# Kernel tuning notes

Hardware: AMD Instinct MI355X
Metric: run time of the kernel (lower is better)

The kernel has to match this reference:

```python
import jax, jax.numpy as jnp
import numpy as np

D_MODEL = 2048
N_HEADS = 16
QK_HEAD_DIM = D_MODEL // N_HEADS  # 128
V_HEAD_DIM = 128
KV_LORA_RANK = 512
EPS = 1e-6
B, S = 2, 2048
ROPE_THETA = 10000.0


def setup_inputs() -> dict:
    key = jax.random.key(0)
    ks = jax.random.split(key, 7)
    x = jax.random.normal(ks[0], (B, S, D_MODEL), dtype=jnp.float32)
    # RoPE frequencies: freqs_cis[s, i] = exp(1j * s * theta^(-2i/d)) -> cos/sin
    inv_freq = 1.0 / (ROPE_THETA ** (np.arange(0, QK_HEAD_DIM, 2, dtype=np.float32) / QK_HEAD_DIM))
    ang = np.arange(S, dtype=np.float32)[:, None] * inv_freq[None, :]  # [S, 64]
    freqs_cos = jnp.asarray(np.cos(ang), dtype=jnp.float32)
    freqs_sin = jnp.asarray(np.sin(ang), dtype=jnp.float32)
    # Parameters stored as [in, out] so that y = x @ W
    def lin(k, fan_in, fan_out):
        return jax.random.normal(k, (fan_in, fan_out), dtype=jnp.float32) / np.sqrt(fan_in)
    w_kv_compress = lin(ks[1], D_MODEL, KV_LORA_RANK)
    kv_norm_w = jnp.ones((KV_LORA_RANK,), dtype=jnp.float32)
    w_k_up = lin(ks[2], KV_LORA_RANK, N_HEADS * QK_HEAD_DIM)
    w_v_up = lin(ks[3], KV_LORA_RANK, N_HEADS * V_HEAD_DIM)
    w_q = lin(ks[4], D_MODEL, N_HEADS * QK_HEAD_DIM)
    w_out = lin(ks[5], N_HEADS * V_HEAD_DIM, D_MODEL)
    return {"x": x, "freqs_cos": freqs_cos, "freqs_sin": freqs_sin,
            "w_kv_compress": w_kv_compress, "kv_norm_w": kv_norm_w,
            "w_k_up": w_k_up, "w_v_up": w_v_up, "w_q": w_q, "w_out": w_out}


def _rms_norm(x, w, eps=EPS):
    var = jnp.mean(jnp.square(x), axis=-1, keepdims=True)
    return x * jax.lax.rsqrt(var + eps) * w


def _apply_rope(t, cos, sin):
    # t: [B, S, H, D]; cos/sin: [S, D//2]; pairs are adjacent elements (complex view)
    b, s, h, d = t.shape
    tr = t.reshape(b, s, h, d // 2, 2)
    x1, x2 = tr[..., 0], tr[..., 1]
    c = cos[None, :, None, :]
    sn = sin[None, :, None, :]
    o1 = x1 * c - x2 * sn
    o2 = x1 * sn + x2 * c
    return jnp.stack([o1, o2], axis=-1).reshape(b, s, h, d)


def reference(x, freqs_cos, freqs_sin, w_kv_compress, kv_norm_w, w_k_up, w_v_up, w_q, w_out):
    b, s, _ = x.shape
    kv_latent = _rms_norm(x @ w_kv_compress, kv_norm_w)      # [B,S,R]
    k = (kv_latent @ w_k_up).reshape(b, s, N_HEADS, QK_HEAD_DIM)
    v = (kv_latent @ w_v_up).reshape(b, s, N_HEADS, V_HEAD_DIM)
    q = (x @ w_q).reshape(b, s, N_HEADS, QK_HEAD_DIM)
    q = _apply_rope(q, freqs_cos, freqs_sin)
    k = _apply_rope(k, freqs_cos, freqs_sin)
    scale = 1.0 / np.sqrt(QK_HEAD_DIM)
    scores = jnp.einsum('bqhd,bkhd->bhqk', q, k) * scale     # [B,H,S,S]
    causal = jnp.tril(jnp.ones((s, s), dtype=bool))
    scores = jnp.where(causal[None, None], scores, jnp.finfo(scores.dtype).min)
    probs = jax.nn.softmax(scores, axis=-1)
    attn = jnp.einsum('bhqk,bkhd->bqhd', probs, v)           # [B,S,H,Dv]
    out = attn.reshape(b, s, N_HEADS * V_HEAD_DIM) @ w_out   # [B,S,d_model]
    return out
```

## Files before the change

### kernel.cpp

```cpp
#include <hip/hip_runtime.h>

typedef unsigned short u16;
typedef __attribute__((ext_vector_type(8))) short bf16x8;
typedef __attribute__((ext_vector_type(4))) float floatx4;

__device__ __forceinline__ float bf2f(u16 h) {
  return __uint_as_float(((unsigned int)h) << 16);
}
__device__ __forceinline__ u16 f2bf(float f) {
  unsigned int u = __float_as_uint(f);
  u += 0x7fffu + ((u >> 16) & 1u);
  return (u16)(u >> 16);
}
__device__ __forceinline__ u16 f2bf_hu(float f) {
  return (u16)((__float_as_uint(f) + 0x8000u) >> 16);
}
__device__ __forceinline__ float exp2fast(float x) {
  float r;
  asm("v_exp_f32 %0, %1" : "=v"(r) : "v"(x));
  return r;
}
__device__ __forceinline__ bool is_f32(const u16* probe) { return probe[0] == 0; }

#define GLOAD_LDS16(gsrc, ldst)                                                        \
  __builtin_amdgcn_global_load_lds(                                                    \
      (const __attribute__((address_space(1))) unsigned int*)(gsrc),                   \
      (__attribute__((address_space(3))) unsigned int*)(ldst), 16, 0, 0)

__global__ __launch_bounds__(256) void cvt_to_bf16(const void* __restrict__ in,
                                                   u16* __restrict__ out, int n,
                                                   const u16* __restrict__ probe) {
  int i = (blockIdx.x * 256 + threadIdx.x) * 8;
  if (i >= n) return;
  if (is_f32(probe)) {
    const float* f = (const float*)in;
    uint4 o;
    o.x = (unsigned)f2bf(f[i + 0]) | ((unsigned)f2bf(f[i + 1]) << 16);
    o.y = (unsigned)f2bf(f[i + 2]) | ((unsigned)f2bf(f[i + 3]) << 16);
    o.z = (unsigned)f2bf(f[i + 4]) | ((unsigned)f2bf(f[i + 5]) << 16);
    o.w = (unsigned)f2bf(f[i + 6]) | ((unsigned)f2bf(f[i + 7]) << 16);
    *(uint4*)(out + i) = o;
  } else {
    *(uint4*)(out + i) = *(const uint4*)((const u16*)in + i);
  }
}

__global__ __launch_bounds__(256) void transpose_cvt(const void* __restrict__ in,
                                                     u16* __restrict__ out,
                                                     int R, int C,
                                                     const u16* __restrict__ probe) {
  __shared__ u16 tile[32][33];
  int bx = blockIdx.x * 32;
  int by = blockIdx.y * 32;
  int tx = threadIdx.x & 31, ty = threadIdx.x >> 5;
  if (is_f32(probe)) {
    const float* f = (const float*)in;
    for (int i = 0; i < 32; i += 8)
      tile[ty + i][tx] = f2bf(f[(size_t)(by + ty + i) * C + (bx + tx)]);
  } else {
    const u16* u = (const u16*)in;
    for (int i = 0; i < 32; i += 8)
      tile[ty + i][tx] = u[(size_t)(by + ty + i) * C + (bx + tx)];
  }
  __syncthreads();
  for (int i = 0; i < 32; i += 8)
    out[(size_t)(bx + ty + i) * R + (by + tx)] = tile[tx][ty + i];
}

__global__ __launch_bounds__(512, 2) void gemm8(const u16* __restrict__ A,
                                                const u16* __restrict__ BT,
                                                void* __restrict__ Ca, int sa,
                                                u16* __restrict__ Cb, int sb,
                                                int N, int K, int nsplit, int mode,
                                                const u16* __restrict__ fc,
                                                const u16* __restrict__ fs,
                                                float oscale,
                                                const u16* __restrict__ probe) {
  extern __shared__ __align__(16) u16 ldsbuf[];
  u16* const AsB = ldsbuf;
  u16* const BsB = ldsbuf + 32768;
#define ASLOT(b, k) (AsB + ((((b) << 1) | (k)) << 13))
#define BSLOT(b, k) (BsB + ((((b) << 1) | (k)) << 13))

  const int t = threadIdx.x;
  const int lane = t & 63, wid = t >> 6;
  const int quad = lane >> 4, l16 = lane & 15;
  const int wr = wid >> 2, wc = wid & 3;
  const int m0 = blockIdx.y * 256, n0 = blockIdx.x * 256;
  const int NT = K >> 6;

  const u16* const Abase = A + (size_t)m0 * K;
  const u16* const Bbase = BT + (size_t)n0 * K;

  const int e0 = t, e1 = 512 + t;
  const int r0 = e0 >> 2, r1 = e1 >> 2;
  const int sg0 = (e0 & 3) ^ ((r0 & 3) ^ ((r0 >> 2) & 3));
  const int sg1 = (e1 & 3) ^ ((r1 & 3) ^ ((r1 >> 2) & 3));
  const u16* const sa0 = Abase + (size_t)r0 * K + sg0 * 8;
  const u16* const sa1 = Abase + (size_t)r1 * K + sg1 * 8;
  const u16* const sb0 = Bbase + (size_t)r0 * K + sg0 * 8;
  const u16* const sb1 = Bbase + (size_t)r1 * K + sg1 * 8;
#define STAGE_A(slot, kb)                      \
  do {                                         \
    GLOAD_LDS16(sa0 + (kb), (slot) + e0 * 8);  \
    GLOAD_LDS16(sa1 + (kb), (slot) + e1 * 8);  \
  } while (0)
#define STAGE_B(slot, kb)                      \
  do {                                         \
    GLOAD_LDS16(sb0 + (kb), (slot) + e0 * 8);  \
    GLOAD_LDS16(sb1 + (kb), (slot) + e1 * 8);  \
  } while (0)

  const int gofs = (quad ^ ((l16 & 3) ^ ((l16 >> 2) & 3))) * 8;
#define FRAG(slot, row) (*(const bf16x8*)((slot) + (row) * 32 + gofs))

#define SYNC_MID()                                          \
  __builtin_amdgcn_s_barrier();                             \
  asm volatile("s_waitcnt lgkmcnt(0)" ::: "memory");        \
  __builtin_amdgcn_sched_barrier(0)

  floatx4 acc[8][4];
#pragma unroll
  for (int i = 0; i < 8; ++i)
#pragma unroll
    for (int j = 0; j < 4; ++j) acc[i][j] = (floatx4){0.f, 0.f, 0.f, 0.f};

  STAGE_A(ASLOT(0, 0), 0);
  STAGE_B(BSLOT(0, 0), 0);
  STAGE_A(ASLOT(0, 1), 32);
  STAGE_B(BSLOT(0, 1), 32);
  STAGE_A(ASLOT(1, 0), 64);
  STAGE_B(BSLOT(1, 0), 64);
  asm volatile("s_waitcnt vmcnt(4)" ::: "memory");
  __builtin_amdgcn_s_barrier();

  bf16x8 af[4], bfr[4];
  const int arow = wr * 128 + l16;
  const int brow = wc * 64 + l16;

#pragma unroll 1
  for (int u = 0; u < NT; ++u) {
    const int cur = u & 1, oth = cur ^ 1;
    u16* const A0 = ASLOT(cur, 0);
    u16* const A1 = ASLOT(cur, 1);
    u16* const B0 = BSLOT(cur, 0);
    u16* const B1 = BSLOT(cur, 1);
    const bool s1 = (u + 1 < NT), s2 = (u + 2 < NT);
    const int kb1 = (u + 1) << 6, kb2 = (u + 2) << 6;

#pragma unroll
    for (int mi = 0; mi < 4; ++mi) af[mi] = FRAG(A0, arow + mi * 16);
#pragma unroll
    for (int nj = 0; nj < 4; ++nj) bfr[nj] = FRAG(B0, brow + nj * 16);
    if (s1) STAGE_A(ASLOT(oth, 1), kb1 + 32);
    SYNC_MID();
    __builtin_amdgcn_s_setprio(1);
#pragma unroll
    for (int mi = 0; mi < 4; ++mi)
#pragma unroll
      for (int nj = 0; nj < 4; ++nj)
        acc[mi][nj] = __builtin_amdgcn_mfma_f32_16x16x32_bf16(af[mi], bfr[nj], acc[mi][nj], 0, 0, 0);
    __builtin_amdgcn_s_setprio(0);
    __builtin_amdgcn_sched_barrier(0);
    __builtin_amdgcn_s_barrier();

#pragma unroll
    for (int mi = 0; mi < 4; ++mi) af[mi] = FRAG(A0, arow + 64 + mi * 16);
    if (s1) STAGE_B(BSLOT(oth, 1), kb1 + 32);
    SYNC_MID();
    __builtin_amdgcn_s_setprio(1);
#pragma unroll
    for (int mi = 0; mi < 4; ++mi)
#pragma unroll
      for (int nj = 0; nj < 4; ++nj)
        acc[mi + 4][nj] = __builtin_amdgcn_mfma_f32_16x16x32_bf16(af[mi], bfr[nj], acc[mi + 4][nj], 0, 0, 0);
    __builtin_amdgcn_s_setprio(0);
    __builtin_amdgcn_sched_barrier(0);
    if (u == NT - 1) asm volatile("s_waitcnt vmcnt(0)" ::: "memory");
    __builtin_amdgcn_s_barrier();

#pragma unroll
    for (int mi = 0; mi < 4; ++mi) af[mi] = FRAG(A1, arow + mi * 16);
#pragma unroll
    for (int nj = 0; nj < 4; ++nj) bfr[nj] = FRAG(B1, brow + nj * 16);
    if (s2) STAGE_A(A0, kb2);
    SYNC_MID();
    __builtin_amdgcn_s_setprio(1);
#pragma unroll
    for (int mi = 0; mi < 4; ++mi)
#pragma unroll
      for (int nj = 0; nj < 4; ++nj)
        acc[mi][nj] = __builtin_amdgcn_mfma_f32_16x16x32_bf16(af[mi], bfr[nj], acc[mi][nj], 0, 0, 0);
    __builtin_amdgcn_s_setprio(0);
    __builtin_amdgcn_sched_barrier(0);
    __builtin_amdgcn_s_barrier();

#pragma unroll
    for (int mi = 0; mi < 4; ++mi) af[mi] = FRAG(A1, arow + 64 + mi * 16);
    if (s2) STAGE_B(B0, kb2);
    SYNC_MID();
    __builtin_amdgcn_s_setprio(1);
#pragma unroll
    for (int mi = 0; mi < 4; ++mi)
#pragma unroll
      for (int nj = 0; nj < 4; ++nj)
        acc[mi + 4][nj] = __builtin_amdgcn_mfma_f32_16x16x32_bf16(af[mi], bfr[nj], acc[mi + 4][nj], 0, 0, 0);
    __builtin_amdgcn_s_setprio(0);
    __builtin_amdgcn_sched_barrier(0);
    asm volatile("s_waitcnt vmcnt(4)" ::: "memory");
    __builtin_amdgcn_s_barrier();
  }

  if (mode == 0) {
    const bool f32o = is_f32(probe);
#pragma unroll
    for (int mi = 0; mi < 8; ++mi) {
      int rbase = m0 + wr * 128 + mi * 16 + quad * 4;
#pragma unroll
      for (int nj = 0; nj < 4; ++nj) {
        int col = n0 + wc * 64 + nj * 16 + l16;
        if (f32o) {
          float* Cf = (float*)Ca;
          for (int r = 0; r < 4; ++r) Cf[(size_t)(rbase + r) * sa + col] = acc[mi][nj][r];
        } else {
          u16* Ch = (u16*)Ca;
          for (int r = 0; r < 4; ++r) Ch[(size_t)(rbase + r) * sa + col] = f2bf(acc[mi][nj][r]);
        }
      }
    }
  } else if (n0 < nsplit) {
    const bool odd = (l16 & 1);
    u16* Ch = (u16*)Ca;
#pragma unroll
    for (int mi = 0; mi < 8; ++mi) {
      int rbase = m0 + wr * 128 + mi * 16 + quad * 4;
#pragma unroll
      for (int nj = 0; nj < 4; ++nj) {
        int col = n0 + wc * 64 + nj * 16 + l16;
        int p = (col & 127) >> 1;
        for (int r = 0; r < 4; ++r) {
          int srow = (rbase + r) & 2047;
          float c = bf2f(fc[srow * 64 + p]);
          float sn = bf2f(fs[srow * 64 + p]);
          float v = acc[mi][nj][r];
          float pv = __shfl_xor(v, 1);
          float o = fmaf(v, c, odd ? pv * sn : -pv * sn);
          Ch[(size_t)(rbase + r) * sa + col] = f2bf(o * oscale);
        }
      }
    }
  } else if (mode == 1) {
#pragma unroll
    for (int mi = 0; mi < 8; ++mi) {
      int rbase = m0 + wr * 128 + mi * 16 + quad * 4;
#pragma unroll
      for (int nj = 0; nj < 4; ++nj) {
        int col = n0 - nsplit + wc * 64 + nj * 16 + l16;
        for (int r = 0; r < 4; ++r)
          Cb[(size_t)(rbase + r) * sb + col] = f2bf(acc[mi][nj][r]);
      }
    }
  } else {
#pragma unroll
    for (int mi = 0; mi < 8; ++mi) {
      int token0 = m0 + wr * 128 + mi * 16 + quad * 4;
#pragma unroll
      for (int nj = 0; nj < 4; ++nj) {
        int ch = n0 - nsplit + wc * 64 + nj * 16 + l16;
        size_t base = (((size_t)((token0 >> 11) * 16 + (ch >> 7)) * 128 + (ch & 127)) << 11) +
                      (token0 & 2047);
        ushort4 pk;
        pk.x = f2bf(acc[mi][nj][0]);
        pk.y = f2bf(acc[mi][nj][1]);
        pk.z = f2bf(acc[mi][nj][2]);
        pk.w = f2bf(acc[mi][nj][3]);
        *(ushort4*)(Cb + base) = pk;
      }
    }
  }
#undef ASLOT
#undef BSLOT
#undef STAGE_A
#undef STAGE_B
#undef FRAG
#undef SYNC_MID
}

__global__ __launch_bounds__(256) void rmsnorm_kernel(u16* __restrict__ t,
                                                      const u16* __restrict__ w) {
  int row = blockIdx.x * 4 + (threadIdx.x >> 6);
  int lane = threadIdx.x & 63;
  u16* xr = t + (size_t)row * 512;
  float v[8];
  float ss = 0.f;
  for (int i = 0; i < 8; ++i) {
    v[i] = bf2f(xr[lane + i * 64]);
    ss += v[i] * v[i];
  }
  for (int d = 32; d > 0; d >>= 1) ss += __shfl_xor(ss, d);
  float r = rsqrtf(ss * (1.f / 512.f) + 1e-6f);
  for (int i = 0; i < 8; ++i) xr[lane + i * 64] = f2bf(v[i] * r * bf2f(w[lane + i * 64]));
}

__global__ __launch_bounds__(256) void attn_kernel(const u16* __restrict__ q,
                                                   const u16* __restrict__ k,
                                                   const u16* __restrict__ vt,
                                                   u16* __restrict__ o) {
  const int S = 2048;
  __shared__ __align__(16) u16 Kt[64 * 128];
  __shared__ __align__(16) u16 Vt[128 * 64];
  __shared__ __align__(16) u16 P[4][16][64];
  const int t = threadIdx.x;
  const int w = t >> 6, lane = t & 63;
  const int quad = lane >> 4, l16 = lane & 15;
  const int bh = blockIdx.x;
  const int b = bh >> 4, h = bh & 15;
  const int qb = (int)gridDim.y - 1 - (int)blockIdx.y;
  const int q0 = qb * 64 + w * 16;

  const u16* qbase = q + ((size_t)(b * S + q0 + l16)) * 2048 + h * 128;
  bf16x8 qf[4];
  for (int c = 0; c < 4; ++c) qf[c] = *(const bf16x8*)(qbase + c * 32 + quad * 8);

  const u16* kbase = k + (size_t)b * S * 2048 + h * 128;
  const u16* vtb = vt + (size_t)bh * 128 * S;

  const int ksrow = t >> 4, ksc = t & 15;
  const int vsrow = t >> 3, vsc = t & 7;

  bf16x8 onesf;
#pragma unroll
  for (int i = 0; i < 8; ++i) onesf[i] = (short)0x3F80;

  float m_i[4], l_i[4];
  floatx4 acc[8];
  for (int r = 0; r < 4; ++r) { m_i[r] = -1e30f; l_i[r] = 0.f; }
  for (int nd = 0; nd < 8; ++nd) acc[nd] = (floatx4){0.f, 0.f, 0.f, 0.f};

  const int kmax = q0 + 15;
  const int qbase64 = qb * 64;
  for (int kb = 0; kb <= qbase64; kb += 64) {
    const bool diag = (kb == qbase64);
    __syncthreads();
    for (int j = 0; j < 4; ++j) {
      int row = j * 16 + ksrow;
      GLOAD_LDS16(kbase + (size_t)(kb + row) * 2048 + (ksc ^ (row & 15)) * 8,
                  Kt + (size_t)(row * 16 + ksc) * 8);
    }
    for (int j = 0; j < 4; ++j) {
      int row = j * 32 + vsrow;
      GLOAD_LDS16(vtb + (size_t)row * S + kb + ((vsc ^ (row & 7)) * 8),
                  Vt + (size_t)(row * 8 + vsc) * 8);
    }
    __syncthreads();

    floatx4 s[4];
    if (!diag) {
      for (int ns = 0; ns < 4; ++ns) {
        s[ns] = (floatx4){0.f, 0.f, 0.f, 0.f};
        for (int c = 0; c < 4; ++c) {
          bf16x8 kf = *(const bf16x8*)&Kt[(ns * 16 + l16) * 128 + ((c * 4 + quad) ^ l16) * 8];
          s[ns] = __builtin_amdgcn_mfma_f32_16x16x32_bf16(qf[c], kf, s[ns], 0, 0, 0);
        }
      }
    } else {
      for (int ns = 0; ns < 4; ++ns) {
        if (kb + ns * 16 <= kmax) {
          s[ns] = (floatx4){0.f, 0.f, 0.f, 0.f};
          for (int c = 0; c < 4; ++c) {
            bf16x8 kf = *(const bf16x8*)&Kt[(ns * 16 + l16) * 128 + ((c * 4 + quad) ^ l16) * 8];
            s[ns] = __builtin_amdgcn_mfma_f32_16x16x32_bf16(qf[c], kf, s[ns], 0, 0, 0);
          }
          int key = kb + ns * 16 + l16;
          for (int r = 0; r < 4; ++r)
            s[ns][r] = (key > q0 + quad * 4 + r) ? -1e30f : s[ns][r];
        } else {
          s[ns] = (floatx4){-1e30f, -1e30f, -1e30f, -1e30f};
        }
      }
    }
    float tmax[4];
    for (int r = 0; r < 4; ++r) {
      float v = fmaxf(fmaxf(s[0][r], s[1][r]), fmaxf(s[2][r], s[3][r]));
      for (int d = 1; d < 16; d <<= 1) v = fmaxf(v, __shfl_xor(v, d));
      tmax[r] = v;
    }
    bool grow = (tmax[0] > m_i[0] + 8.f) || (tmax[1] > m_i[1] + 8.f) ||
                (tmax[2] > m_i[2] + 8.f) || (tmax[3] > m_i[3] + 8.f);
    if (__any(grow)) {
      for (int r = 0; r < 4; ++r) {
        float mn = fmaxf(m_i[r], tmax[r]);
        float alpha = exp2fast(m_i[r] - mn);
        m_i[r] = mn;
        l_i[r] *= alpha;
        for (int nd = 0; nd < 8; ++nd) acc[nd][r] *= alpha;
      }
    }
    for (int ns = 0; ns < 4; ++ns)
      for (int r = 0; r < 4; ++r) s[ns][r] = exp2fast(s[ns][r] - m_i[r]);
    for (int ns = 0; ns < 4; ++ns)
      for (int r = 0; r < 4; ++r) {
        int row = quad * 4 + r;
        P[w][row][(((ns * 2 + (l16 >> 3)) ^ (row & 7)) << 3) | (l16 & 7)] = f2bf_hu(s[ns][r]);
      }
    floatx4 ls = (floatx4){0.f, 0.f, 0.f, 0.f};
    for (int kc = 0; kc < 2; ++kc) {
      if (!diag || kb + kc * 32 <= kmax) {
        bf16x8 pa = *(const bf16x8*)&P[w][l16][((kc * 4 + quad) ^ (l16 & 7)) * 8];
        ls = __builtin_amdgcn_mfma_f32_16x16x32_bf16(pa, onesf, ls, 0, 0, 0);
        for (int nd = 0; nd < 8; ++nd) {
          int d = nd * 16 + l16;
          bf16x8 vf = *(const bf16x8*)&Vt[(d * 8 + ((kc * 4 + quad) ^ (d & 7))) * 8];
          acc[nd] = __builtin_amdgcn_mfma_f32_16x16x32_bf16(pa, vf, acc[nd], 0, 0, 0);
        }
      }
    }
    for (int r = 0; r < 4; ++r) l_i[r] += ls[r];
  }
  u16* ob = o + ((size_t)(b * S + q0 + quad * 4)) * 2048 + h * 128;
  for (int r = 0; r < 4; ++r) {
    float inv = 1.f / l_i[r];
    for (int nd = 0; nd < 8; ++nd)
      ob[(size_t)r * 2048 + nd * 16 + l16] = f2bf(acc[nd][r] * inv);
  }
}

extern "C" void kernel_launch(void* const* d_in, const int* in_sizes, int n_in,
                              void* d_out, int out_size, void* d_ws, size_t ws_size,
                              hipStream_t stream) {
  const void* x    = d_in[0];
  const void* fcos = d_in[1];
  const void* fsin = d_in[2];
  const void* wkv  = d_in[3];
  const void* wnr  = d_in[4];
  const void* wku  = d_in[5];
  const void* wvu  = d_in[6];
  const void* wq   = d_in[7];
  const void* wo   = d_in[8];
  const u16* probe = (const u16*)fcos;

  const size_t MB = 1u << 20;
  char* ws = (char*)d_ws;
  u16* xc    = (u16*)(ws);
  u16* vtb   = (u16*)(ws);
  u16* qb    = (u16*)(ws + 16 * MB);
  u16* kb    = (u16*)(ws + 32 * MB);
  u16* ab    = (u16*)(ws + 48 * MB);
  u16* lat   = (u16*)(ws + 64 * MB);
  u16* wqT   = (u16*)(ws + 68 * MB);
  u16* woT   = (u16*)(ws + 68 * MB);
  u16* wkvT  = (u16*)(ws + 76 * MB);
  u16* wkT   = (u16*)(ws + 78 * MB);
  u16* wvT   = (u16*)(ws + 80 * MB);
  u16* fcosc = (u16*)(ws + 82 * MB);
  u16* fsinc = (u16*)(ws + 82 * MB + 256 * 1024);
  u16* wnrc  = (u16*)(ws + 82 * MB + 512 * 1024);

  const float QSCALE = 0.08838834764831845f * 1.4426950408889634f;
  dim3 blk(256);

  hipFuncSetAttribute((const void*)gemm8, hipFuncAttributeMaxDynamicSharedMemorySize,
                      131072);

  cvt_to_bf16<<<dim3(4096), blk, 0, stream>>>(x, xc, 8388608, probe);
  cvt_to_bf16<<<dim3(64), blk, 0, stream>>>(fcos, fcosc, 131072, probe);
  cvt_to_bf16<<<dim3(64), blk, 0, stream>>>(fsin, fsinc, 131072, probe);
  cvt_to_bf16<<<dim3(1), blk, 0, stream>>>(wnr, wnrc, 512, probe);

  transpose_cvt<<<dim3(64, 64), blk, 0, stream>>>(wq, wqT, 2048, 2048, probe);
  transpose_cvt<<<dim3(16, 64), blk, 0, stream>>>(wkv, wkvT, 2048, 512, probe);

  gemm8<<<dim3(10, 16), dim3(512), 131072, stream>>>(xc, wqT, qb, 2048, lat, 512,
                                                     2560, 2048, 2048, 1,
                                                     fcosc, fsinc, QSCALE, probe);
  rmsnorm_kernel<<<dim3(1024), blk, 0, stream>>>(lat, wnrc);

  transpose_cvt<<<dim3(64, 16), blk, 0, stream>>>(wku, wkT, 512, 2048, probe);
  transpose_cvt<<<dim3(64, 16), blk, 0, stream>>>(wvu, wvT, 512, 2048, probe);
  gemm8<<<dim3(16, 16), dim3(512), 131072, stream>>>(lat, wkT, kb, 2048, vtb, 0,
                                                     4096, 512, 2048, 2,
                                                     fcosc, fsinc, 1.0f, probe);

  transpose_cvt<<<dim3(64, 64), blk, 0, stream>>>(wo, woT, 2048, 2048, probe);

  attn_kernel<<<dim3(32, 32), blk, 0, stream>>>(qb, kb, vtb, ab);

  gemm8<<<dim3(8, 16), dim3(512), 131072, stream>>>(ab, woT, d_out, 2048, nullptr, 0,
                                                    2048, 2048, 0, 0,
                                                    nullptr, nullptr, 1.0f, probe);
}
```

Measured before the change: 389.3 us.

## Shrink GEMM block tile to 256x128 with 4x2 warp layout

Changes the GEMM kernel from 256x256 tiles with 2x4 warps (each 128x64) to 256x128 tiles with 4x2 warps (each 64x64), halving B staging and LDS use and doubling the grid for all three projections. The goal is more blocks to fill the CUs (the grids were only 128-256 blocks) and lower LDS and register pressure. The K-loop is restructured so each half-tile does one MFMA batch with a single barrier pair, and the vmcnt waits are adjusted. The cost is lower arithmetic intensity per block, so global and L2 traffic for A rises.

```diff
diff --git a/kernel.cpp b/kernel.cpp
--- a/kernel.cpp
+++ b/kernel.cpp
@@ -67,49 +67,44 @@
     out[(size_t)(bx + ty + i) * R + (by + tx)] = tile[tx][ty + i];
 }
 
-__global__ __launch_bounds__(512, 2) void gemm8(const u16* __restrict__ A,
-                                                const u16* __restrict__ BT,
-                                                void* __restrict__ Ca, int sa,
-                                                u16* __restrict__ Cb, int sb,
-                                                int N, int K, int nsplit, int mode,
-                                                const u16* __restrict__ fc,
-                                                const u16* __restrict__ fs,
-                                                float oscale,
-                                                const u16* __restrict__ probe) {
+__global__ __launch_bounds__(512, 2) void gemm28(const u16* __restrict__ A,
+                                                 const u16* __restrict__ BT,
+                                                 void* __restrict__ Ca, int sa,
+                                                 u16* __restrict__ Cb, int sb,
+                                                 int N, int K, int nsplit, int mode,
+                                                 const u16* __restrict__ fc,
+                                                 const u16* __restrict__ fs,
+                                                 float oscale,
+                                                 const u16* __restrict__ probe) {
   extern __shared__ __align__(16) u16 ldsbuf[];
   u16* const AsB = ldsbuf;
   u16* const BsB = ldsbuf + 32768;
 #define ASLOT(b, k) (AsB + ((((b) << 1) | (k)) << 13))
-#define BSLOT(b, k) (BsB + ((((b) << 1) | (k)) << 13))
+#define BSLOT(b, k) (BsB + ((((b) << 1) | (k)) << 12))
 
   const int t = threadIdx.x;
   const int lane = t & 63, wid = t >> 6;
   const int quad = lane >> 4, l16 = lane & 15;
-  const int wr = wid >> 2, wc = wid & 3;
-  const int m0 = blockIdx.y * 256, n0 = blockIdx.x * 256;
+  const int wr = wid >> 1, wc = wid & 1;
+  const int m0 = blockIdx.y * 256, n0 = blockIdx.x * 128;
   const int NT = K >> 6;
 
   const u16* const Abase = A + (size_t)m0 * K;
   const u16* const Bbase = BT + (size_t)n0 * K;
 
   const int e0 = t, e1 = 512 + t;
-  const int r0 = e0 >> 2, r1 = e1 >> 2;
-  const int sg0 = (e0 & 3) ^ ((r0 & 3) ^ ((r0 >> 2) & 3));
-  const int sg1 = (e1 & 3) ^ ((r1 & 3) ^ ((r1 >> 2) & 3));
-  const u16* const sa0 = Abase + (size_t)r0 * K + sg0 * 8;
-  const u16* const sa1 = Abase + (size_t)r1 * K + sg1 * 8;
-  const u16* const sb0 = Bbase + (size_t)r0 * K + sg0 * 8;
-  const u16* const sb1 = Bbase + (size_t)r1 * K + sg1 * 8;
+  const int ra0 = e0 >> 2, ra1 = e1 >> 2;
+  const int sg0 = (e0 & 3) ^ ((ra0 & 3) ^ ((ra0 >> 2) & 3));
+  const int sg1 = (e1 & 3) ^ ((ra1 & 3) ^ ((ra1 >> 2) & 3));
+  const u16* const sa0 = Abase + (size_t)ra0 * K + sg0 * 8;
+  const u16* const sa1 = Abase + (size_t)ra1 * K + sg1 * 8;
+  const u16* const sb0 = Bbase + (size_t)ra0 * K + sg0 * 8;
 #define STAGE_A(slot, kb)                      \
   do {                                         \
     GLOAD_LDS16(sa0 + (kb), (slot) + e0 * 8);  \
     GLOAD_LDS16(sa1 + (kb), (slot) + e1 * 8);  \
   } while (0)
-#define STAGE_B(slot, kb)                      \
-  do {                                         \
-    GLOAD_LDS16(sb0 + (kb), (slot) + e0 * 8);  \
-    GLOAD_LDS16(sb1 + (kb), (slot) + e1 * 8);  \
-  } while (0)
+#define STAGE_B(slot, kb) GLOAD_LDS16(sb0 + (kb), (slot) + e0 * 8)
 
   const int gofs = (quad ^ ((l16 & 3) ^ ((l16 >> 2) & 3))) * 8;
 #define FRAG(slot, row) (*(const bf16x8*)((slot) + (row) * 32 + gofs))
@@ -119,9 +114,9 @@
   asm volatile("s_waitcnt lgkmcnt(0)" ::: "memory");        \
   __builtin_amdgcn_sched_barrier(0)
 
-  floatx4 acc[8][4];
-#pragma unroll
-  for (int i = 0; i < 8; ++i)
+  floatx4 acc[4][4];
+#pragma unroll
+  for (int i = 0; i < 4; ++i)
 #pragma unroll
     for (int j = 0; j < 4; ++j) acc[i][j] = (floatx4){0.f, 0.f, 0.f, 0.f};
 
@@ -131,28 +126,27 @@
   STAGE_B(BSLOT(0, 1), 32);
   STAGE_A(ASLOT(1, 0), 64);
   STAGE_B(BSLOT(1, 0), 64);
-  asm volatile("s_waitcnt vmcnt(4)" ::: "memory");
+  asm volatile("s_waitcnt vmcnt(3)" ::: "memory");
   __builtin_amdgcn_s_barrier();
 
   bf16x8 af[4], bfr[4];
-  const int arow = wr * 128 + l16;
+  const int arow = wr * 64 + l16;
   const int brow = wc * 64 + l16;
 
 #pragma unroll 1
   for (int u = 0; u < NT; ++u) {
     const int cur = u & 1, oth = cur ^ 1;
-    u16* const A0 = ASLOT(cur, 0);
-    u16* const A1 = ASLOT(cur, 1);
-    u16* const B0 = BSLOT(cur, 0);
-    u16* const B1 = BSLOT(cur, 1);
     const bool s1 = (u + 1 < NT), s2 = (u + 2 < NT);
     const int kb1 = (u + 1) << 6, kb2 = (u + 2) << 6;
 
 #pragma unroll
-    for (int mi = 0; mi < 4; ++mi) af[mi] = FRAG(A0, arow + mi * 16);
-#pragma unroll
-    for (int nj = 0; nj < 4; ++nj) bfr[nj] = FRAG(B0, brow + nj * 16);
-    if (s1) STAGE_A(ASLOT(oth, 1), kb1 + 32);
+    for (int mi = 0; mi < 4; ++mi) af[mi] = FRAG(ASLOT(cur, 0), arow + mi * 16);
+#pragma unroll
+    for (int nj = 0; nj < 4; ++nj) bfr[nj] = FRAG(BSLOT(cur, 0), brow + nj * 16);
+    if (s1) {
+      STAGE_A(ASLOT(oth, 1), kb1 + 32);
+      STAGE_B(BSLOT(oth, 1), kb1 + 32);
+    }
     SYNC_MID();
     __builtin_amdgcn_s_setprio(1);
 #pragma unroll
@@ -165,25 +159,13 @@
     __builtin_amdgcn_s_barrier();
 
 #pragma unroll
-    for (int mi = 0; mi < 4; ++mi) af[mi] = FRAG(A0, arow + 64 + mi * 16);
-    if (s1) STAGE_B(BSLOT(oth, 1), kb1 + 32);
-    SYNC_MID();
-    __builtin_amdgcn_s_setprio(1);
-#pragma unroll
-    for (int mi = 0; mi < 4; ++mi)
-#pragma unroll
-      for (int nj = 0; nj < 4; ++nj)
-        acc[mi + 4][nj] = __builtin_amdgcn_mfma_f32_16x16x32_bf16(af[mi], bfr[nj], acc[mi + 4][nj], 0, 0, 0);
-    __builtin_amdgcn_s_setprio(0);
-    __builtin_amdgcn_sched_barrier(0);
-    if (u == NT - 1) asm volatile("s_waitcnt vmcnt(0)" ::: "memory");
-    __builtin_amdgcn_s_barrier();
-
-#pragma unroll
-    for (int mi = 0; mi < 4; ++mi) af[mi] = FRAG(A1, arow + mi * 16);
-#pragma unroll
-    for (int nj = 0; nj < 4; ++nj) bfr[nj] = FRAG(B1, brow + nj * 16);
-    if (s2) STAGE_A(A0, kb2);
+    for (int mi = 0; mi < 4; ++mi) af[mi] = FRAG(ASLOT(cur, 1), arow + mi * 16);
+#pragma unroll
+    for (int nj = 0; nj < 4; ++nj) bfr[nj] = FRAG(BSLOT(cur, 1), brow + nj * 16);
+    if (s2) {
+      STAGE_A(ASLOT(cur, 0), kb2);
+      STAGE_B(BSLOT(cur, 0), kb2);
+    }
     SYNC_MID();
     __builtin_amdgcn_s_setprio(1);
 #pragma unroll
@@ -193,29 +175,18 @@
         acc[mi][nj] = __builtin_amdgcn_mfma_f32_16x16x32_bf16(af[mi], bfr[nj], acc[mi][nj], 0, 0, 0);
     __builtin_amdgcn_s_setprio(0);
     __builtin_amdgcn_sched_barrier(0);
-    __builtin_amdgcn_s_barrier();
-
-#pragma unroll
-    for (int mi = 0; mi < 4; ++mi) af[mi] = FRAG(A1, arow + 64 + mi * 16);
-    if (s2) STAGE_B(B0, kb2);
-    SYNC_MID();
-    __builtin_amdgcn_s_setprio(1);
-#pragma unroll
-    for (int mi = 0; mi < 4; ++mi)
-#pragma unroll
-      for (int nj = 0; nj < 4; ++nj)
-        acc[mi + 4][nj] = __builtin_amdgcn_mfma_f32_16x16x32_bf16(af[mi], bfr[nj], acc[mi + 4][nj], 0, 0, 0);
-    __builtin_amdgcn_s_setprio(0);
-    __builtin_amdgcn_sched_barrier(0);
-    asm volatile("s_waitcnt vmcnt(4)" ::: "memory");
+    if (s2)
+      asm volatile("s_waitcnt vmcnt(3)" ::: "memory");
+    else
+      asm volatile("s_waitcnt vmcnt(0)" ::: "memory");
     __builtin_amdgcn_s_barrier();
   }
 
   if (mode == 0) {
     const bool f32o = is_f32(probe);
 #pragma unroll
-    for (int mi = 0; mi < 8; ++mi) {
-      int rbase = m0 + wr * 128 + mi * 16 + quad * 4;
+    for (int mi = 0; mi < 4; ++mi) {
+      int rbase = m0 + wr * 64 + mi * 16 + quad * 4;
 #pragma unroll
       for (int nj = 0; nj < 4; ++nj) {
         int col = n0 + wc * 64 + nj * 16 + l16;
@@ -232,8 +203,8 @@
     const bool odd = (l16 & 1);
     u16* Ch = (u16*)Ca;
 #pragma unroll
-    for (int mi = 0; mi < 8; ++mi) {
-      int rbase = m0 + wr * 128 + mi * 16 + quad * 4;
+    for (int mi = 0; mi < 4; ++mi) {
+      int rbase = m0 + wr * 64 + mi * 16 + quad * 4;
 #pragma unroll
       for (int nj = 0; nj < 4; ++nj) {
         int col = n0 + wc * 64 + nj * 16 + l16;
@@ -251,8 +222,8 @@
     }
   } else if (mode == 1) {
 #pragma unroll
-    for (int mi = 0; mi < 8; ++mi) {
-      int rbase = m0 + wr * 128 + mi * 16 + quad * 4;
+    for (int mi = 0; mi < 4; ++mi) {
+      int rbase = m0 + wr * 64 + mi * 16 + quad * 4;
 #pragma unroll
       for (int nj = 0; nj < 4; ++nj) {
         int col = n0 - nsplit + wc * 64 + nj * 16 + l16;
@@ -262,8 +233,8 @@
     }
   } else {
 #pragma unroll
-    for (int mi = 0; mi < 8; ++mi) {
-      int token0 = m0 + wr * 128 + mi * 16 + quad * 4;
+    for (int mi = 0; mi < 4; ++mi) {
+      int token0 = m0 + wr * 64 + mi * 16 + quad * 4;
 #pragma unroll
       for (int nj = 0; nj < 4; ++nj) {
         int ch = n0 - nsplit + wc * 64 + nj * 16 + l16;
@@ -459,8 +430,8 @@
   const float QSCALE = 0.08838834764831845f * 1.4426950408889634f;
   dim3 blk(256);
 
-  hipFuncSetAttribute((const void*)gemm8, hipFuncAttributeMaxDynamicSharedMemorySize,
-                      131072);
+  hipFuncSetAttribute((const void*)gemm28, hipFuncAttributeMaxDynamicSharedMemorySize,
+                      98304);
 
   cvt_to_bf16<<<dim3(4096), blk, 0, stream>>>(x, xc, 8388608, probe);
   cvt_to_bf16<<<dim3(64), blk, 0, stream>>>(fcos, fcosc, 131072, probe);
@@ -470,14 +441,14 @@
   transpose_cvt<<<dim3(64, 64), blk, 0, stream>>>(wq, wqT, 2048, 2048, probe);
   transpose_cvt<<<dim3(16, 64), blk, 0, stream>>>(wkv, wkvT, 2048, 512, probe);
 
-  gemm8<<<dim3(10, 16), dim3(512), 131072, stream>>>(xc, wqT, qb, 2048, lat, 512,
+  gemm28<<<dim3(20, 16), dim3(512), 98304, stream>>>(xc, wqT, qb, 2048, lat, 512,
                                                      2560, 2048, 2048, 1,
                                                      fcosc, fsinc, QSCALE, probe);
   rmsnorm_kernel<<<dim3(1024), blk, 0, stream>>>(lat, wnrc);
 
   transpose_cvt<<<dim3(64, 16), blk, 0, stream>>>(wku, wkT, 512, 2048, probe);
   transpose_cvt<<<dim3(64, 16), blk, 0, stream>>>(wvu, wvT, 512, 2048, probe);
-  gemm8<<<dim3(16, 16), dim3(512), 131072, stream>>>(lat, wkT, kb, 2048, vtb, 0,
+  gemm28<<<dim3(32, 16), dim3(512), 98304, stream>>>(lat, wkT, kb, 2048, vtb, 0,
                                                      4096, 512, 2048, 2,
                                                      fcosc, fsinc, 1.0f, probe);
 
@@ -485,7 +456,7 @@
 
   attn_kernel<<<dim3(32, 32), blk, 0, stream>>>(qb, kb, vtb, ab);
 
-  gemm8<<<dim3(8, 16), dim3(512), 131072, stream>>>(ab, woT, d_out, 2048, nullptr, 0,
-                                                    2048, 2048, 0, 0,
-                                                    nullptr, nullptr, 1.0f, probe);
-}
+  gemm28<<<dim3(16, 16), dim3(512), 98304, stream>>>(ab, woT, d_out, 2048, nullptr, 0,
+                                                     2048, 2048, 0, 0,
+                                                     nullptr, nullptr, 1.0f, probe);
+}
```

Measured after the change: 386.9 us. About the same (-0.6%).
